# Performance work log

Hardware: AMD Instinct MI355X
Metric: run time of the kernel (lower is better)

## Reference

```python
import jax, jax.numpy as jnp
import numpy as np

B, L, V, E = 4096, 200, 100000, 50  # users, max ratings per user, movie vocab, embedding size


def setup_inputs() -> dict:
    key = jax.random.key(0)
    ks = jax.random.split(key, 10)
    emb = jax.random.normal(ks[0], (V, E), jnp.float32) * 0.1
    user_movie_idx = jax.random.randint(ks[1], (B, L), 0, V)
    lengths = jax.random.randint(ks[2], (B,), 1, L + 1)  # at least 1 rating per user
    ratings = jax.random.uniform(ks[3], (B, L), jnp.float32, 0.5, 5.0)
    movie_idx = jax.random.randint(ks[4], (B,), 0, V)

    def lin(k, fan_in, fan_out):
        bound = 1.0 / np.sqrt(fan_in)
        return jax.random.uniform(k, (fan_in, fan_out), jnp.float32, -bound, bound)

    W1 = lin(ks[5], 5 * E, 2 * E)
    b1 = jnp.zeros((2 * E,), jnp.float32)
    W2 = lin(ks[6], 2 * E, E)
    b2 = jnp.zeros((E,), jnp.float32)
    W3 = lin(ks[7], E, 1)
    b3 = jnp.zeros((1,), jnp.float32)
    return dict(emb=emb, ratings=ratings, W1=W1, b1=b1, W2=W2, b2=b2, W3=W3, b3=b3,
                user_movie_idx=user_movie_idx, lengths=lengths, movie_idx=movie_idx)


def reference(emb, ratings, W1, b1, W2, b2, W3, b3, user_movie_idx, lengths, movie_idx):
    # ragged per-user weighted gather: [B, L, E]
    mask = (jnp.arange(L)[None, :] < lengths[:, None])  # [B, L] valid positions
    w = emb[user_movie_idx] * ratings[:, :, None]
    m = mask[:, :, None]
    inf = jnp.float32(jnp.inf)

    wmin = jnp.min(jnp.where(m, w, inf), axis=1)          # [B, E]
    wmax = jnp.max(jnp.where(m, w, -inf), axis=1)         # [B, E]
    n = lengths[:, None].astype(w.dtype)
    wmean = jnp.sum(jnp.where(m, w, 0.0), axis=1) / n     # [B, E]
    # torch median = lower median: sorted index (n-1)//2; pad with +inf so it sorts last
    ws = jnp.sort(jnp.where(m, w, inf), axis=1)
    med_idx = jnp.broadcast_to(((lengths - 1) // 2)[:, None, None], (B, 1, E))
    wmed = jnp.take_along_axis(ws, med_idx, axis=1)[:, 0, :]  # [B, E]

    u = jnp.concatenate([wmin, wmax, wmean, wmed], axis=1)  # [B, 4E]
    u = u / jnp.linalg.norm(u, axis=1, keepdims=True)

    x = jnp.concatenate([u, emb[movie_idx]], axis=1)        # [B, 5E]
    h = jax.nn.relu(x @ W1 + b1)   # dropout is identity in eval
    h = jax.nn.relu(h @ W2 + b2)
    return jax.nn.sigmoid(h @ W3 + b3)  # [B, 1]
```

## Files before the change

kernel.cpp:

```cpp
#include <hip/hip_runtime.h>
#include <math.h>

#define NB 4096
#define LL 200
#define EE 50
#define CH 104
#define CP 105
#define NT 512
#define GG 8
#define IT 25
#define IT1 13
#define SW 8

__device__ __forceinline__ unsigned f2key(float f) {
    unsigned b = __float_as_uint(f);
    unsigned mask = (b & 0x80000000u) ? 0xFFFFFFFFu : 0x80000000u;
    return b ^ mask;
}
__device__ __forceinline__ float key2f(unsigned kk) {
    unsigned mask = (kk & 0x80000000u) ? 0x80000000u : 0xFFFFFFFFu;
    return __uint_as_float(kk ^ mask);
}

__device__ __forceinline__ unsigned select_median(
    int n, int k, int g, int grp, const unsigned it[IT],
    unsigned kmin, unsigned kmax, unsigned (*sbuf)[SW], int *scnt)
{
    unsigned LO = kmin, HI = kmax + 1u;
    int cLO = 0, cHI = n;
    unsigned med = 0u;
    bool small = false;
    int pass = 0;
    for (;;) {
        if (HI - LO == 1u) { med = LO; break; }
        const int w = cHI - cLO;
        if (w <= SW) { small = true; break; }
        unsigned P;
        if (pass < 8) {
            const float vlo = key2f(LO);
            const float vhi = key2f(HI - 1u);
            const float frac = (float)(k - cLO + 1) / (float)(w + 1);
            P = f2key(vlo + (vhi - vlo) * frac);
        } else {
            P = LO + ((HI - LO) >> 1);
        }
        if (P <= LO) P = LO + 1u;
        if (P >= HI) P = HI - 1u;
        int c = 0;
        #pragma unroll
        for (int t = 0; t < IT; t++) c += (it[t] < P) ? 1 : 0;
        c += __shfl_xor(c, 1);
        c += __shfl_xor(c, 2);
        c += __shfl_xor(c, 4);
        if (c > k) { HI = P; cHI = c; }
        else       { LO = P; cLO = c; }
        pass++;
    }
    if (small) {
        const int w = cHI - cLO;
        const int r = k - cLO;
        #pragma unroll
        for (int t = 0; t < IT; t++) {
            const unsigned kk = it[t];
            if (kk >= LO && kk < HI) {
                const int pos = atomicAdd(&scnt[grp], 1);
                if (pos < SW) sbuf[grp][pos] = kk;
            }
        }
        const unsigned sv = (g < w) ? sbuf[grp][g] : 0xFFFFFFFFu;
        int cLess = 0, cLeq = 0;
        for (int j = 0; j < w; j++) {
            const unsigned o = sbuf[grp][j];
            cLess += (o <  sv) ? 1 : 0;
            cLeq  += (o <= sv) ? 1 : 0;
        }
        unsigned cand = (g < w && cLess <= r && r < cLeq) ? sv : 0xFFFFFFFFu;
        #pragma unroll
        for (int m2 = 1; m2 < GG; m2 <<= 1)
            cand = min(cand, (unsigned)__shfl_xor((int)cand, m2));
        med = cand;
    }
    return med;
}

extern "C" __global__ void __launch_bounds__(NT, 8)
rec_fused(const float* __restrict__ emb, const float* __restrict__ ratings,
          const float* __restrict__ W1, const float* __restrict__ b1,
          const float* __restrict__ W2, const float* __restrict__ b2,
          const float* __restrict__ W3, const float* __restrict__ b3,
          const int* __restrict__ uidx, const int* __restrict__ lens,
          const int* __restrict__ midx, float* __restrict__ out)
{
    __shared__ unsigned wK[EE][CP];
    __shared__ int      idxL[LL];
    __shared__ float    ratL[LL];
    __shared__ unsigned sbuf[NT/GG][SW];
    __shared__ int      scnt[NT/GG];
    __shared__ float    u[4*EE];
    __shared__ float    xs[5*EE];
    __shared__ float    h1s[2*EE];

    const int b   = blockIdx.x;
    const int tid = threadIdx.x;
    const int n   = lens[b];
    const int k   = (n - 1) >> 1;

    if (tid < NT/GG) scnt[tid] = 0;
    if (tid < n) {
        idxL[tid] = uidx[b*LL + tid];
        ratL[tid] = ratings[b*LL + tid];
    }
    __syncthreads();

    const int f = tid >> 3;
    const int g = tid & 7;

    const int c1 = (n < CH) ? n : CH;
    for (int p = tid; p < c1*(EE/2); p += NT) {
        const int l  = p / (EE/2);
        const int e2 = p - l*(EE/2);
        const float2 ev = ((const float2*)emb)[(size_t)idxL[l]*(EE/2) + e2];
        const float  r  = ratL[l];
        wK[2*e2    ][l] = f2key(ev.x * r);
        wK[2*e2 + 1][l] = f2key(ev.y * r);
    }
    __syncthreads();

    unsigned it[IT];
    unsigned kmin = 0xFFFFFFFFu, kmax = 0u;
    float sm = 0.f;
    if (f < EE) {
        #pragma unroll
        for (int t = 0; t < IT1; t++) {
            const int l = g + (t << 3);
            unsigned kk = 0xFFFFFFFFu;
            if (l < n) {
                kk = wK[f][l];
                kmin = min(kmin, kk); kmax = max(kmax, kk); sm += key2f(kk);
            }
            it[t] = kk;
        }
    }
    __syncthreads();

    const int c2 = n - CH;
    for (int p = tid; p < c2*(EE/2); p += NT) {
        const int col = p / (EE/2);
        const int e2  = p - col*(EE/2);
        const int l   = CH + col;
        const float2 ev = ((const float2*)emb)[(size_t)idxL[l]*(EE/2) + e2];
        const float  r  = ratL[l];
        wK[2*e2    ][col] = f2key(ev.x * r);
        wK[2*e2 + 1][col] = f2key(ev.y * r);
    }
    __syncthreads();

    if (f < EE) {
        #pragma unroll
        for (int t = IT1; t < IT; t++) {
            const int l = g + (t << 3);
            unsigned kk = 0xFFFFFFFFu;
            if (l < n) {
                kk = wK[f][l - CH];
                kmin = min(kmin, kk); kmax = max(kmax, kk); sm += key2f(kk);
            }
            it[t] = kk;
        }
        #pragma unroll
        for (int m2 = 1; m2 < GG; m2 <<= 1) {
            kmin = min(kmin, (unsigned)__shfl_xor((int)kmin, m2));
            kmax = max(kmax, (unsigned)__shfl_xor((int)kmax, m2));
            sm  += __shfl_xor(sm, m2);
        }

        const unsigned med = select_median(n, k, g, f, it, kmin, kmax,
                                           sbuf, scnt);
        if (g == 0) {
            u[f]        = key2f(kmin);
            u[EE + f]   = key2f(kmax);
            u[2*EE + f] = sm / (float)n;
            u[3*EE + f] = key2f(med);
        }
    }
    __syncthreads();

    if (tid < 64) {
        const int lane = tid;

        const float uv0 = u[lane];
        const float uv1 = u[lane + 64];
        const float uv2 = u[lane + 128];
        const float uv3 = (lane < 4*EE - 192) ? u[lane + 192] : 0.f;
        float v2 = uv0*uv0 + uv1*uv1 + uv2*uv2 + uv3*uv3;
        #pragma unroll
        for (int m2 = 1; m2 < 64; m2 <<= 1) v2 += __shfl_xor(v2, m2);
        const float inv = 1.0f / sqrtf(v2);

        xs[lane]       = uv0 * inv;
        xs[lane + 64]  = uv1 * inv;
        xs[lane + 128] = uv2 * inv;
        if (lane < 4*EE - 192) xs[lane + 192] = uv3 * inv;
        if (lane < EE) xs[4*EE + lane] = emb[(size_t)midx[b]*EE + lane];
        asm volatile("s_waitcnt lgkmcnt(0)" ::: "memory");

        const int o2 = (lane + 64 < 2*EE) ? lane + 64 : 2*EE - 1;
        float a0 = 0.f, a1 = 0.f;
        #pragma unroll 5
        for (int i = 0; i < 5*EE; i++) {
            const float xv = xs[i];
            a0 += xv * W1[i*(2*EE) + lane];
            a1 += xv * W1[i*(2*EE) + o2];
        }
        const float h0  = fmaxf(a0 + b1[lane], 0.f);
        const float h64 = fmaxf(a1 + b1[o2],   0.f);
        h1s[lane] = h0;
        if (lane < 2*EE - 64) h1s[lane + 64] = h64;
        asm volatile("s_waitcnt lgkmcnt(0)" ::: "memory");

        const int oc = (lane < EE) ? lane : EE - 1;
        float a2 = 0.f;
        #pragma unroll 5
        for (int i = 0; i < 2*EE; i++)
            a2 += h1s[i] * W2[i*EE + oc];
        const float h2v = fmaxf(a2 + b2[oc], 0.f);
        float v = (lane < EE) ? h2v * W3[lane] : 0.f;
        #pragma unroll
        for (int m2 = 1; m2 < 64; m2 <<= 1) v += __shfl_xor(v, m2);
        if (lane == 0) out[b] = 1.0f / (1.0f + expf(-(v + b3[0])));
    }
}

extern "C" void kernel_launch(void* const* d_in, const int* in_sizes, int n_in,
                              void* d_out, int out_size, void* d_ws, size_t ws_size,
                              hipStream_t stream) {
    const float* emb     = (const float*)d_in[0];
    const float* ratings = (const float*)d_in[1];
    const float* W1      = (const float*)d_in[2];
    const float* b1      = (const float*)d_in[3];
    const float* W2      = (const float*)d_in[4];
    const float* b2      = (const float*)d_in[5];
    const float* W3      = (const float*)d_in[6];
    const float* b3      = (const float*)d_in[7];
    const int*   uidx    = (const int*)d_in[8];
    const int*   lens    = (const int*)d_in[9];
    const int*   midx    = (const int*)d_in[10];
    float* out = (float*)d_out;

    hipLaunchKernelGGL(rec_fused, dim3(NB), dim3(NT), 0, stream,
                       emb, ratings, W1, b1, W2, b2, W3, b3, uidx, lens, midx, out);
}
```

Measured before the change: 103.3 us.

## Split MLP into consumer blocks synchronized via global counters with producer stat blocks

```diff
diff --git a/kernel.cpp b/kernel.cpp
--- a/kernel.cpp
+++ b/kernel.cpp
@@ -11,6 +11,10 @@
 #define IT 25
 #define IT1 13
 #define SW 8
+#define K2B 256
+#define BPB 16
+
+__device__ int g_done[K2B];
 
 __device__ __forceinline__ unsigned f2key(float f) {
     unsigned b = __float_as_uint(f);
@@ -21,6 +25,21 @@
     unsigned mask = (kk & 0x80000000u) ? 0x80000000u : 0xFFFFFFFFu;
     return __uint_as_float(kk ^ mask);
 }
+
+struct ProdS {
+    unsigned wK[EE][CP];
+    int      idxL[LL];
+    float    ratL[LL];
+    unsigned sbuf[EE][SW];
+    int      scnt[EE];
+};
+struct ConsS {
+    float W2s[2*EE*EE];
+    float b1s[2*EE];
+    float b2s[EE];
+    float W3s[EE];
+    float xs[8][252];
+};
 
 __device__ __forceinline__ unsigned select_median(
     int n, int k, int g, int grp, const unsigned it[IT],
@@ -89,144 +108,168 @@
           const float* __restrict__ W2, const float* __restrict__ b2,
           const float* __restrict__ W3, const float* __restrict__ b3,
           const int* __restrict__ uidx, const int* __restrict__ lens,
-          const int* __restrict__ midx, float* __restrict__ out)
+          const int* __restrict__ midx, float* __restrict__ uo,
+          float* __restrict__ out)
 {
-    __shared__ unsigned wK[EE][CP];
-    __shared__ int      idxL[LL];
-    __shared__ float    ratL[LL];
-    __shared__ unsigned sbuf[NT/GG][SW];
-    __shared__ int      scnt[NT/GG];
-    __shared__ float    u[4*EE];
-    __shared__ float    xs[5*EE];
-    __shared__ float    h1s[2*EE];
-
-    const int b   = blockIdx.x;
+    __shared__ union US { ProdS p; ConsS c; } sm;
+    const int bid = blockIdx.x;
     const int tid = threadIdx.x;
-    const int n   = lens[b];
-    const int k   = (n - 1) >> 1;
-
-    if (tid < NT/GG) scnt[tid] = 0;
-    if (tid < n) {
-        idxL[tid] = uidx[b*LL + tid];
-        ratL[tid] = ratings[b*LL + tid];
-    }
-    __syncthreads();
-
-    const int f = tid >> 3;
-    const int g = tid & 7;
-
-    const int c1 = (n < CH) ? n : CH;
-    for (int p = tid; p < c1*(EE/2); p += NT) {
-        const int l  = p / (EE/2);
-        const int e2 = p - l*(EE/2);
-        const float2 ev = ((const float2*)emb)[(size_t)idxL[l]*(EE/2) + e2];
-        const float  r  = ratL[l];
-        wK[2*e2    ][l] = f2key(ev.x * r);
-        wK[2*e2 + 1][l] = f2key(ev.y * r);
-    }
-    __syncthreads();
-
-    unsigned it[IT];
-    unsigned kmin = 0xFFFFFFFFu, kmax = 0u;
-    float sm = 0.f;
-    if (f < EE) {
+
+    if (bid < NB) {
+        const int b = bid;
+        const int n = lens[b];
+        const int k = (n - 1) >> 1;
+
+        if (tid < EE) sm.p.scnt[tid] = 0;
+        if (tid < n) {
+            sm.p.idxL[tid] = uidx[b*LL + tid];
+            sm.p.ratL[tid] = ratings[b*LL + tid];
+        }
+        __syncthreads();
+
+        const int f = tid >> 3;
+        const int g = tid & 7;
+
+        const int c1 = (n < CH) ? n : CH;
+        for (int p = tid; p < c1*(EE/2); p += NT) {
+            const int l  = p / (EE/2);
+            const int e2 = p - l*(EE/2);
+            const float2 ev = ((const float2*)emb)[(size_t)sm.p.idxL[l]*(EE/2) + e2];
+            const float  r  = sm.p.ratL[l];
+            sm.p.wK[2*e2    ][l] = f2key(ev.x * r);
+            sm.p.wK[2*e2 + 1][l] = f2key(ev.y * r);
+        }
+        __syncthreads();
+
+        unsigned it[IT];
+        unsigned kmin = 0xFFFFFFFFu, kmax = 0u;
+        float smm = 0.f;
+        if (f < EE) {
+            #pragma unroll
+            for (int t = 0; t < IT1; t++) {
+                const int l = g + (t << 3);
+                unsigned kk = 0xFFFFFFFFu;
+                if (l < n) {
+                    kk = sm.p.wK[f][l];
+                    kmin = min(kmin, kk); kmax = max(kmax, kk);
+                    smm += key2f(kk);
+                }
+                it[t] = kk;
+            }
+        }
+        __syncthreads();
+
+        const int c2 = n - CH;
+        for (int p = tid; p < c2*(EE/2); p += NT) {
+            const int col = p / (EE/2);
+            const int e2  = p - col*(EE/2);
+            const int l   = CH + col;
+            const float2 ev = ((const float2*)emb)[(size_t)sm.p.idxL[l]*(EE/2) + e2];
+            const float  r  = sm.p.ratL[l];
+            sm.p.wK[2*e2    ][col] = f2key(ev.x * r);
+            sm.p.wK[2*e2 + 1][col] = f2key(ev.y * r);
+        }
+        __syncthreads();
+
+        if (f < EE) {
+            #pragma unroll
+            for (int t = IT1; t < IT; t++) {
+                const int l = g + (t << 3);
+                unsigned kk = 0xFFFFFFFFu;
+                if (l < n) {
+                    kk = sm.p.wK[f][l - CH];
+                    kmin = min(kmin, kk); kmax = max(kmax, kk);
+                    smm += key2f(kk);
+                }
+                it[t] = kk;
+            }
+            #pragma unroll
+            for (int m2 = 1; m2 < GG; m2 <<= 1) {
+                kmin = min(kmin, (unsigned)__shfl_xor((int)kmin, m2));
+                kmax = max(kmax, (unsigned)__shfl_xor((int)kmax, m2));
+                smm += __shfl_xor(smm, m2);
+            }
+
+            const unsigned med = select_median(n, k, g, f, it, kmin, kmax,
+                                               sm.p.sbuf, sm.p.scnt);
+            if (g == 0) {
+                float* ub = uo + (size_t)b * (4*EE);
+                ub[f]        = key2f(kmin);
+                ub[EE + f]   = key2f(kmax);
+                ub[2*EE + f] = smm / (float)n;
+                ub[3*EE + f] = key2f(med);
+            }
+        }
+        __syncthreads();
+        if (tid == 0)
+            __hip_atomic_fetch_add(&g_done[b >> 4], 1,
+                                   __ATOMIC_RELEASE, __HIP_MEMORY_SCOPE_AGENT);
+    } else {
+        const int j = bid - NB;
+
+        for (int p = tid; p < (2*EE*EE)/2; p += NT)
+            ((float2*)sm.c.W2s)[p] = ((const float2*)W2)[p];
+        if (tid < 2*EE) sm.c.b1s[tid] = b1[tid];
+        if (tid < EE)   { sm.c.b2s[tid] = b2[tid]; sm.c.W3s[tid] = W3[tid]; }
+
+        if (tid == 0) {
+            while (__hip_atomic_load(&g_done[j], __ATOMIC_ACQUIRE,
+                                     __HIP_MEMORY_SCOPE_AGENT) < BPB)
+                __builtin_amdgcn_s_sleep(8);
+        }
+        __syncthreads();
+        const float bias3 = b3[0];
+
+        const int w    = tid >> 6;
+        const int lane = tid & 63;
+
         #pragma unroll
-        for (int t = 0; t < IT1; t++) {
-            const int l = g + (t << 3);
-            unsigned kk = 0xFFFFFFFFu;
-            if (l < n) {
-                kk = wK[f][l];
-                kmin = min(kmin, kk); kmax = max(kmax, kk); sm += key2f(kk);
-            }
-            it[t] = kk;
-        }
-    }
-    __syncthreads();
-
-    const int c2 = n - CH;
-    for (int p = tid; p < c2*(EE/2); p += NT) {
-        const int col = p / (EE/2);
-        const int e2  = p - col*(EE/2);
-        const int l   = CH + col;
-        const float2 ev = ((const float2*)emb)[(size_t)idxL[l]*(EE/2) + e2];
-        const float  r  = ratL[l];
-        wK[2*e2    ][col] = f2key(ev.x * r);
-        wK[2*e2 + 1][col] = f2key(ev.y * r);
-    }
-    __syncthreads();
-
-    if (f < EE) {
-        #pragma unroll
-        for (int t = IT1; t < IT; t++) {
-            const int l = g + (t << 3);
-            unsigned kk = 0xFFFFFFFFu;
-            if (l < n) {
-                kk = wK[f][l - CH];
-                kmin = min(kmin, kk); kmax = max(kmax, kk); sm += key2f(kk);
-            }
-            it[t] = kk;
-        }
-        #pragma unroll
-        for (int m2 = 1; m2 < GG; m2 <<= 1) {
-            kmin = min(kmin, (unsigned)__shfl_xor((int)kmin, m2));
-            kmax = max(kmax, (unsigned)__shfl_xor((int)kmax, m2));
-            sm  += __shfl_xor(sm, m2);
-        }
-
-        const unsigned med = select_median(n, k, g, f, it, kmin, kmax,
-                                           sbuf, scnt);
-        if (g == 0) {
-            u[f]        = key2f(kmin);
-            u[EE + f]   = key2f(kmax);
-            u[2*EE + f] = sm / (float)n;
-            u[3*EE + f] = key2f(med);
-        }
-    }
-    __syncthreads();
-
-    if (tid < 64) {
-        const int lane = tid;
-
-        const float uv0 = u[lane];
-        const float uv1 = u[lane + 64];
-        const float uv2 = u[lane + 128];
-        const float uv3 = (lane < 4*EE - 192) ? u[lane + 192] : 0.f;
-        float v2 = uv0*uv0 + uv1*uv1 + uv2*uv2 + uv3*uv3;
-        #pragma unroll
-        for (int m2 = 1; m2 < 64; m2 <<= 1) v2 += __shfl_xor(v2, m2);
-        const float inv = 1.0f / sqrtf(v2);
-
-        xs[lane]       = uv0 * inv;
-        xs[lane + 64]  = uv1 * inv;
-        xs[lane + 128] = uv2 * inv;
-        if (lane < 4*EE - 192) xs[lane + 192] = uv3 * inv;
-        if (lane < EE) xs[4*EE + lane] = emb[(size_t)midx[b]*EE + lane];
-        asm volatile("s_waitcnt lgkmcnt(0)" ::: "memory");
-
-        const int o2 = (lane + 64 < 2*EE) ? lane + 64 : 2*EE - 1;
-        float a0 = 0.f, a1 = 0.f;
-        #pragma unroll 5
-        for (int i = 0; i < 5*EE; i++) {
-            const float xv = xs[i];
-            a0 += xv * W1[i*(2*EE) + lane];
-            a1 += xv * W1[i*(2*EE) + o2];
-        }
-        const float h0  = fmaxf(a0 + b1[lane], 0.f);
-        const float h64 = fmaxf(a1 + b1[o2],   0.f);
-        h1s[lane] = h0;
-        if (lane < 2*EE - 64) h1s[lane + 64] = h64;
-        asm volatile("s_waitcnt lgkmcnt(0)" ::: "memory");
-
-        const int oc = (lane < EE) ? lane : EE - 1;
-        float a2 = 0.f;
-        #pragma unroll 5
-        for (int i = 0; i < 2*EE; i++)
-            a2 += h1s[i] * W2[i*EE + oc];
-        const float h2v = fmaxf(a2 + b2[oc], 0.f);
-        float v = (lane < EE) ? h2v * W3[lane] : 0.f;
-        #pragma unroll
-        for (int m2 = 1; m2 < 64; m2 <<= 1) v += __shfl_xor(v, m2);
-        if (lane == 0) out[b] = 1.0f / (1.0f + expf(-(v + b3[0])));
+        for (int rep = 0; rep < 2; rep++) {
+            const int b = j * BPB + rep * 8 + w;
+
+            const float* ub = uo + (size_t)b * (4*EE);
+            const float uv0 = ub[lane];
+            const float uv1 = ub[lane + 64];
+            const float uv2 = ub[lane + 128];
+            const float uv3 = (lane < 4*EE - 192) ? ub[lane + 192] : 0.f;
+            float v2 = uv0*uv0 + uv1*uv1 + uv2*uv2 + uv3*uv3;
+            #pragma unroll
+            for (int m2 = 1; m2 < 64; m2 <<= 1) v2 += __shfl_xor(v2, m2);
+            const float inv = 1.0f / sqrtf(v2);
+
+            sm.c.xs[w][lane]       = uv0 * inv;
+            sm.c.xs[w][lane + 64]  = uv1 * inv;
+            sm.c.xs[w][lane + 128] = uv2 * inv;
+            if (lane < 4*EE - 192) sm.c.xs[w][lane + 192] = uv3 * inv;
+            if (lane < EE)
+                sm.c.xs[w][4*EE + lane] = emb[(size_t)midx[b]*EE + lane];
+            asm volatile("s_waitcnt lgkmcnt(0)" ::: "memory");
+
+            const int o2 = (lane + 64 < 2*EE) ? lane + 64 : 2*EE - 1;
+            float a0 = 0.f, a1 = 0.f;
+            #pragma unroll 5
+            for (int i = 0; i < 5*EE; i++) {
+                const float xv = sm.c.xs[w][i];
+                a0 += xv * W1[i*(2*EE) + lane];
+                a1 += xv * W1[i*(2*EE) + o2];
+            }
+            const float h0  = fmaxf(a0 + sm.c.b1s[lane], 0.f);
+            const float h64 = fmaxf(a1 + sm.c.b1s[o2],   0.f);
+            sm.c.xs[w][lane] = h0;
+            if (lane < 2*EE - 64) sm.c.xs[w][lane + 64] = h64;
+            asm volatile("s_waitcnt lgkmcnt(0)" ::: "memory");
+
+            const int oc = (lane < EE) ? lane : EE - 1;
+            float a2 = 0.f;
+            #pragma unroll 5
+            for (int i = 0; i < 2*EE; i++)
+                a2 += sm.c.xs[w][i] * sm.c.W2s[i*EE + oc];
+            const float h2v = fmaxf(a2 + sm.c.b2s[oc], 0.f);
+            float v = (lane < EE) ? h2v * sm.c.W3s[lane] : 0.f;
+            #pragma unroll
+            for (int m2 = 1; m2 < 64; m2 <<= 1) v += __shfl_xor(v, m2);
+            if (lane == 0) out[b] = 1.0f / (1.0f + expf(-(v + bias3)));
+        }
     }
 }
 
@@ -245,7 +288,13 @@
     const int*   lens    = (const int*)d_in[9];
     const int*   midx    = (const int*)d_in[10];
     float* out = (float*)d_out;
-
-    hipLaunchKernelGGL(rec_fused, dim3(NB), dim3(NT), 0, stream,
-                       emb, ratings, W1, b1, W2, b2, W3, b3, uidx, lens, midx, out);
-}
+    float* uo  = (float*)d_ws;
+
+    static void* gsym = nullptr;
+    if (!gsym) hipGetSymbolAddress(&gsym, HIP_SYMBOL(g_done));
+    hipMemsetAsync(gsym, 0, sizeof(int) * K2B, stream);
+
+    hipLaunchKernelGGL(rec_fused, dim3(NB + K2B), dim3(NT), 0, stream,
+                       emb, ratings, W1, b1, W2, b2, W3, b3,
+                       uidx, lens, midx, uo, out);
+}
```

New measurement: 190.7 us. 1.85x slower.
